# Performance work log

Hardware: AMD Instinct MI355X
Metric: run time of the kernel (lower is better)

## Reference

```python
import jax, jax.numpy as jnp
import numpy as np

E, W, S, Q, D = 256, 20, 5, 300, 512
ALPHA = 37.0  # hardcoded weight '37' in computeProto


def setup_inputs() -> dict:
    key = jax.random.key(0)
    k1, k2 = jax.random.split(key)
    x_shot = jax.random.normal(k1, (E, W, S, D), dtype=jnp.float32)
    x_query = jax.random.normal(k2, (E, Q, D), dtype=jnp.float32)
    temp = jnp.float32(10.0)
    return {"x_shot": x_shot, "x_query": x_query, "temp": temp}


def compute_proto(x_shot, x_query):
    # x_shot: [E, W, S, D], x_query: [E, Q, D]
    n_shot = x_shot.shape[2]
    shot_sum = x_shot.sum(axis=2)                      # [E, W, D]
    shot_mean = x_shot.mean(axis=2)                    # [E, W, D]
    # pairwise euclidean distance mean-vs-query: [E, W, Q]
    diff = shot_mean[:, :, None, :] - x_query[:, None, :, :]
    dist = jnp.sqrt(jnp.sum(diff * diff, axis=-1))
    weights = jax.nn.softmax(-dist, axis=-1)           # softmax over queries
    pooled = jnp.einsum('ewq,eqd->ewd', weights, x_query)  # [E, W, D]
    proto = (shot_sum + ALPHA * pooled) / (n_shot + ALPHA)
    return proto


def l2norm(x, axis=-1, eps=1e-12):
    n = jnp.sqrt(jnp.sum(x * x, axis=axis, keepdims=True))
    return x / jnp.maximum(n, eps)


def reference(x_shot, x_query, temp):
    proto = compute_proto(x_shot, x_query)             # [E, W, D]
    proto = l2norm(proto)
    q = l2norm(x_query)
    logits = temp * jnp.einsum('eqd,ewd->eqw', q, proto)  # [E, Q, W]
    return logits
```

## Files before the change

kernel.cpp:

```cpp
#include <hip/hip_runtime.h>
#include <math.h>

#define E_ 256
#define W_ 20
#define S_ 5
#define Q_ 300
#define D_ 512
#define ALPHA_ 37.0f
#define QCH 64
#define NCH 5
#define QPAD 304

typedef __attribute__((ext_vector_type(8))) short bf16x8;
typedef __attribute__((ext_vector_type(4))) float f32x4;
typedef __attribute__((ext_vector_type(4))) unsigned int u32x4;

#define OFF_SS   0
#define OFF_XQ   32768
#define OFF_BUF  98304
#define OFF_Q2   122624
#define OFF_M2   123904
#define OFF_RED  124032
#define LDS_BYTES 124672

__device__ __forceinline__ unsigned short f2bf(float x) {
    unsigned int u = __builtin_bit_cast(unsigned int, x);
    u += 0x7fffu + ((u >> 16) & 1u);
    return (unsigned short)(u >> 16);
}
__device__ __forceinline__ float bf2f(unsigned short h) {
    unsigned int u = ((unsigned int)h) << 16;
    return __builtin_bit_cast(float, u);
}

__device__ __forceinline__ bf16x8 ldfrag(const char* base, int row, int k0) {
    const int phys = (k0 >> 3) ^ (row & 7);
    return *reinterpret_cast<const bf16x8*>(base + row * 1024 + phys * 16);
}

__device__ __forceinline__ void stage_chunk(const float4* xq4, char* s_xq, float* s_q2,
                                            int c, int qcount, int tid, bool write_q2) {
    const int qr = tid >> 3;
    const int i  = tid & 7;
    const bool valid = qr < qcount;
    const int qg = c * QCH + qr;
    float q2 = 0.f;
    const float4* row4 = xq4 + (size_t)(valid ? qg : 0) * (D_ / 4);
    #pragma unroll
    for (int j = 0; j < 8; ++j) {
        const int ch = i + 8 * j;
        float4 a = valid ? row4[2 * ch]     : make_float4(0.f, 0.f, 0.f, 0.f);
        float4 b = valid ? row4[2 * ch + 1] : make_float4(0.f, 0.f, 0.f, 0.f);
        q2 += a.x * a.x + a.y * a.y + a.z * a.z + a.w * a.w
            + b.x * b.x + b.y * b.y + b.z * b.z + b.w * b.w;
        u32x4 v;
        v[0] = (unsigned int)f2bf(a.x) | ((unsigned int)f2bf(a.y) << 16);
        v[1] = (unsigned int)f2bf(a.z) | ((unsigned int)f2bf(a.w) << 16);
        v[2] = (unsigned int)f2bf(b.x) | ((unsigned int)f2bf(b.y) << 16);
        v[3] = (unsigned int)f2bf(b.z) | ((unsigned int)f2bf(b.w) << 16);
        *reinterpret_cast<u32x4*>(s_xq + qr * 1024 + ((ch ^ (qr & 7)) << 4)) = v;
    }
    if (write_q2) {
        q2 += __shfl_xor(q2, 1);
        q2 += __shfl_xor(q2, 2);
        q2 += __shfl_xor(q2, 4);
        if (i == 0) s_q2[qg] = valid ? q2 : 0.f;
    }
}

__global__ __launch_bounds__(512) void fused4(const float* __restrict__ xs,
                                              const float* __restrict__ xq,
                                              const float* __restrict__ temp_p,
                                              float* __restrict__ out) {
    extern __shared__ char smem[];
    char*  s_ss  = smem + OFF_SS;
    char*  s_xq  = smem + OFF_XQ;
    float* s_buf = (float*)(smem + OFF_BUF);
    float* s_q2  = (float*)(smem + OFF_Q2);
    float* s_m2  = (float*)(smem + OFF_M2);
    float* s_red = (float*)(smem + OFF_RED);

    const int e    = blockIdx.x;
    const int tid  = threadIdx.x;
    const int lane = tid & 63;
    const int wv   = tid >> 6;
    const int ln15 = lane & 15;
    const int hi   = lane >> 4;

    const float*  xse = xs + (size_t)e * (W_ * S_ * D_);
    const float*  xqe = xq + (size_t)e * (Q_ * D_);
    const float4* xq4 = (const float4*)xqe;
    const float   temp = *temp_p;

    for (int idx = tid; idx < 12 * 64; idx += 512) {
        const int row = 20 + (idx >> 6), ch = idx & 63;
        u32x4 z = {0u, 0u, 0u, 0u};
        *reinterpret_cast<u32x4*>(s_ss + row * 1024 + ch * 16) = z;
    }
    {
        const int chb = tid >> 3;
        #pragma unroll
        for (int w = 0; w < W_; ++w) {
            float a = 0.f;
            #pragma unroll
            for (int s = 0; s < S_; ++s) a += xse[(w * S_ + s) * D_ + tid];
            *(unsigned short*)(s_ss + w * 1024 + ((chb ^ (w & 7)) << 4) + (tid & 7) * 2) = f2bf(a);
        }
    }
    __syncthreads();

    for (int w = wv; w < W_; w += 8) {
        bf16x8 v = *reinterpret_cast<const bf16x8*>(s_ss + w * 1024 + ((lane ^ (w & 7)) << 4));
        float p = 0.f;
        #pragma unroll
        for (int j = 0; j < 8; ++j) { float f = bf2f((unsigned short)v[j]); p += f * f; }
        #pragma unroll
        for (int off = 32; off; off >>= 1) p += __shfl_xor(p, off);
        if (lane == 0) s_m2[w] = p * (1.f / (S_ * S_));
    }
    __syncthreads();

    for (int c = 0; c < NCH; ++c) {
        const int qcount = (c == 4) ? (Q_ - 4 * QCH) : QCH;
        stage_chunk(xq4, s_xq, s_q2, c, qcount, tid, true);
        __syncthreads();
        const int mtile = wv >> 2, ntile = wv & 3;
        f32x4 acc = {0.f, 0.f, 0.f, 0.f};
        const int arow = mtile * 16 + ln15;
        const int brow = ntile * 16 + ln15;
        #pragma unroll
        for (int k = 0; k < 16; ++k) {
            bf16x8 a = ldfrag(s_ss, arow, k * 32 + hi * 8);
            bf16x8 b = ldfrag(s_xq, brow, k * 32 + hi * 8);
            acc = __builtin_amdgcn_mfma_f32_16x16x32_bf16(a, b, acc, 0, 0, 0);
        }
        const int qloc = ntile * 16 + ln15;
        if (qloc < qcount) {
            const int qg = c * QCH + qloc;
            const float q2v = s_q2[qg];
            #pragma unroll
            for (int r = 0; r < 4; ++r) {
                const int w = mtile * 16 + hi * 4 + r;
                if (w < W_) {
                    float d2 = s_m2[w] + q2v - 0.4f * acc[r];
                    s_buf[w * QPAD + qg] = -sqrtf(fmaxf(d2, 0.f));
                }
            }
        }
        __syncthreads();
    }

    for (int w = wv; w < W_; w += 8) {
        float mx = -1e30f;
        for (int q = lane; q < Q_; q += 64) mx = fmaxf(mx, s_buf[w * QPAD + q]);
        #pragma unroll
        for (int off = 32; off; off >>= 1) mx = fmaxf(mx, __shfl_xor(mx, off));
        float sm = 0.f;
        for (int q = lane; q < Q_; q += 64) {
            float ex = __expf(s_buf[w * QPAD + q] - mx);
            s_buf[w * QPAD + q] = ex;
            sm += ex;
        }
        #pragma unroll
        for (int off = 32; off; off >>= 1) sm += __shfl_xor(sm, off);
        const float inv = 1.f / sm;
        for (int q = lane; q < Q_; q += 64) s_buf[w * QPAD + q] *= inv;
    }
    __syncthreads();

    {
        float pr[W_];
        #pragma unroll
        for (int w = 0; w < W_; ++w) pr[w] = 0.f;
        for (int q0 = 0; q0 < Q_; q0 += 4) {
            const float qv0 = xqe[(q0 + 0) * D_ + tid];
            const float qv1 = xqe[(q0 + 1) * D_ + tid];
            const float qv2 = xqe[(q0 + 2) * D_ + tid];
            const float qv3 = xqe[(q0 + 3) * D_ + tid];
            #pragma unroll
            for (int w = 0; w < W_; ++w) {
                const float4 wt = *reinterpret_cast<const float4*>(&s_buf[w * QPAD + q0]);
                pr[w] += wt.x * qv0 + wt.y * qv1 + wt.z * qv2 + wt.w * qv3;
            }
        }
        const int chb = tid >> 3;
        #pragma unroll
        for (int w = 0; w < W_; ++w) {
            unsigned short h =
                *(unsigned short*)(s_ss + w * 1024 + ((chb ^ (w & 7)) << 4) + (tid & 7) * 2);
            pr[w] = (bf2f(h) + ALPHA_ * pr[w]) * (1.f / (S_ + ALPHA_));
        }
        #pragma unroll
        for (int w = 0; w < W_; ++w) {
            float p = pr[w] * pr[w];
            #pragma unroll
            for (int off = 32; off; off >>= 1) p += __shfl_xor(p, off);
            if (lane == 0) s_red[wv * W_ + w] = p;
        }
        __syncthreads();
        if (tid < W_) {
            float p = 0.f;
            #pragma unroll
            for (int k = 0; k < 8; ++k) p += s_red[k * W_ + tid];
            s_m2[tid] = 1.f / fmaxf(sqrtf(p), 1e-12f);
        }
        __syncthreads();
        #pragma unroll
        for (int w = 0; w < W_; ++w) {
            *(unsigned short*)(s_ss + w * 1024 + ((chb ^ (w & 7)) << 4) + (tid & 7) * 2) =
                f2bf(pr[w] * s_m2[w]);
        }
        __syncthreads();
    }

    for (int c = 0; c < NCH; ++c) {
        const int qcount = (c == 4) ? (Q_ - 4 * QCH) : QCH;
        stage_chunk(xq4, s_xq, s_q2, c, qcount, tid, false);
        __syncthreads();
        const int mtile = wv >> 1, ntile = wv & 1;
        f32x4 acc = {0.f, 0.f, 0.f, 0.f};
        const int arow = mtile * 16 + ln15;
        const int brow = ntile * 16 + ln15;
        #pragma unroll
        for (int k = 0; k < 16; ++k) {
            bf16x8 a = ldfrag(s_xq, arow, k * 32 + hi * 8);
            bf16x8 b = ldfrag(s_ss, brow, k * 32 + hi * 8);
            acc = __builtin_amdgcn_mfma_f32_16x16x32_bf16(a, b, acc, 0, 0, 0);
        }
        const int w = ntile * 16 + ln15;
        if (w < W_) {
            #pragma unroll
            for (int r = 0; r < 4; ++r) {
                const int qloc = mtile * 16 + hi * 4 + r;
                if (qloc < qcount) {
                    const int qg = c * QCH + qloc;
                    const float scale = temp / fmaxf(sqrtf(s_q2[qg]), 1e-12f);
                    out[(size_t)e * (Q_ * W_) + qg * W_ + w] = scale * acc[r];
                }
            }
        }
        __syncthreads();
    }
}

extern "C" void kernel_launch(void* const* d_in, const int* in_sizes, int n_in,
                              void* d_out, int out_size, void* d_ws, size_t ws_size,
                              hipStream_t stream) {
    const float* xs = (const float*)d_in[0];
    const float* xq = (const float*)d_in[1];
    const float* tp = (const float*)d_in[2];
    hipFuncSetAttribute(reinterpret_cast<const void*>(fused4),
                        hipFuncAttributeMaxDynamicSharedMemorySize, LDS_BYTES);
    fused4<<<E_, 512, LDS_BYTES, stream>>>(xs, xq, tp, (float*)d_out);
}
```

Measured before the change: 120.3 us.

## Prefetch next query chunk into registers and vectorize shot-sum loads

```diff
diff --git a/kernel.cpp b/kernel.cpp
--- a/kernel.cpp
+++ b/kernel.cpp
@@ -13,6 +13,7 @@
 
 typedef __attribute__((ext_vector_type(8))) short bf16x8;
 typedef __attribute__((ext_vector_type(4))) float f32x4;
+typedef __attribute__((ext_vector_type(2))) unsigned int u32x2;
 typedef __attribute__((ext_vector_type(4))) unsigned int u32x4;
 
 #define OFF_SS   0
@@ -38,21 +39,36 @@
     return *reinterpret_cast<const bf16x8*>(base + row * 1024 + phys * 16);
 }
 
-__device__ __forceinline__ void stage_chunk(const float4* xq4, char* s_xq, float* s_q2,
-                                            int c, int qcount, int tid, bool write_q2) {
+__device__ __forceinline__ void stage_load(const float4* xq4, int c, int qcount,
+                                           int tid, float4* r) {
+    const int qr = tid >> 3;
+    const int i  = tid & 7;
+    const int qg = c * QCH + ((qr < qcount) ? qr : 0);
+    const float4* row4 = xq4 + (size_t)qg * (D_ / 4);
+    #pragma unroll
+    for (int j = 0; j < 8; ++j) {
+        const int ch = i + 8 * j;
+        r[2 * j]     = row4[2 * ch];
+        r[2 * j + 1] = row4[2 * ch + 1];
+    }
+}
+
+template <bool WQ2>
+__device__ __forceinline__ void stage_write(const float4* r, char* s_xq, float* s_q2,
+                                            int c, int qcount, int tid) {
     const int qr = tid >> 3;
     const int i  = tid & 7;
     const bool valid = qr < qcount;
-    const int qg = c * QCH + qr;
     float q2 = 0.f;
-    const float4* row4 = xq4 + (size_t)(valid ? qg : 0) * (D_ / 4);
     #pragma unroll
     for (int j = 0; j < 8; ++j) {
         const int ch = i + 8 * j;
-        float4 a = valid ? row4[2 * ch]     : make_float4(0.f, 0.f, 0.f, 0.f);
-        float4 b = valid ? row4[2 * ch + 1] : make_float4(0.f, 0.f, 0.f, 0.f);
-        q2 += a.x * a.x + a.y * a.y + a.z * a.z + a.w * a.w
-            + b.x * b.x + b.y * b.y + b.z * b.z + b.w * b.w;
+        float4 a = valid ? r[2 * j]     : make_float4(0.f, 0.f, 0.f, 0.f);
+        float4 b = valid ? r[2 * j + 1] : make_float4(0.f, 0.f, 0.f, 0.f);
+        if (WQ2) {
+            q2 += a.x * a.x + a.y * a.y + a.z * a.z + a.w * a.w
+                + b.x * b.x + b.y * b.y + b.z * b.z + b.w * b.w;
+        }
         u32x4 v;
         v[0] = (unsigned int)f2bf(a.x) | ((unsigned int)f2bf(a.y) << 16);
         v[1] = (unsigned int)f2bf(a.z) | ((unsigned int)f2bf(a.w) << 16);
@@ -60,15 +76,15 @@
         v[3] = (unsigned int)f2bf(b.z) | ((unsigned int)f2bf(b.w) << 16);
         *reinterpret_cast<u32x4*>(s_xq + qr * 1024 + ((ch ^ (qr & 7)) << 4)) = v;
     }
-    if (write_q2) {
+    if (WQ2) {
         q2 += __shfl_xor(q2, 1);
         q2 += __shfl_xor(q2, 2);
         q2 += __shfl_xor(q2, 4);
-        if (i == 0) s_q2[qg] = valid ? q2 : 0.f;
-    }
-}
-
-__global__ __launch_bounds__(512) void fused4(const float* __restrict__ xs,
+        if (i == 0) s_q2[c * QCH + qr] = valid ? q2 : 0.f;
+    }
+}
+
+__global__ __launch_bounds__(512) void fused5(const float* __restrict__ xs,
                                               const float* __restrict__ xq,
                                               const float* __restrict__ temp_p,
                                               float* __restrict__ out) {
@@ -92,20 +108,32 @@
     const float4* xq4 = (const float4*)xqe;
     const float   temp = *temp_p;
 
+    float4 buf[16];
+
+    stage_load(xq4, 0, QCH, tid, buf);
+
     for (int idx = tid; idx < 12 * 64; idx += 512) {
         const int row = 20 + (idx >> 6), ch = idx & 63;
         u32x4 z = {0u, 0u, 0u, 0u};
         *reinterpret_cast<u32x4*>(s_ss + row * 1024 + ch * 16) = z;
     }
-    {
-        const int chb = tid >> 3;
-        #pragma unroll
-        for (int w = 0; w < W_; ++w) {
-            float a = 0.f;
-            #pragma unroll
-            for (int s = 0; s < S_; ++s) a += xse[(w * S_ + s) * D_ + tid];
-            *(unsigned short*)(s_ss + w * 1024 + ((chb ^ (w & 7)) << 4) + (tid & 7) * 2) = f2bf(a);
-        }
+    #pragma unroll
+    for (int it = 0; it < 5; ++it) {
+        const int idx = it * 512 + tid;
+        const int w   = idx >> 7;
+        const int dq  = idx & 127;
+        const float4* p0 = reinterpret_cast<const float4*>(xse + (w * S_) * D_ + dq * 4);
+        float4 a = p0[0];
+        #pragma unroll
+        for (int s = 1; s < S_; ++s) {
+            const float4 t = p0[s * (D_ / 4)];
+            a.x += t.x; a.y += t.y; a.z += t.z; a.w += t.w;
+        }
+        u32x2 v;
+        v[0] = (unsigned int)f2bf(a.x) | ((unsigned int)f2bf(a.y) << 16);
+        v[1] = (unsigned int)f2bf(a.z) | ((unsigned int)f2bf(a.w) << 16);
+        *reinterpret_cast<u32x2*>(s_ss + w * 1024 + (((dq >> 1) ^ (w & 7)) << 4) +
+                                  (dq & 1) * 8) = v;
     }
     __syncthreads();
 
@@ -122,8 +150,11 @@
 
     for (int c = 0; c < NCH; ++c) {
         const int qcount = (c == 4) ? (Q_ - 4 * QCH) : QCH;
-        stage_chunk(xq4, s_xq, s_q2, c, qcount, tid, true);
-        __syncthreads();
+        stage_write<true>(buf, s_xq, s_q2, c, qcount, tid);
+        __syncthreads();
+        if (c + 1 < NCH)
+            stage_load(xq4, c + 1, (c + 1 == 4) ? (Q_ - 4 * QCH) : QCH, tid, buf);
+
         const int mtile = wv >> 2, ntile = wv & 3;
         f32x4 acc = {0.f, 0.f, 0.f, 0.f};
         const int arow = mtile * 16 + ln15;
@@ -168,6 +199,8 @@
     }
     __syncthreads();
 
+    stage_load(xq4, 0, QCH, tid, buf);
+
     {
         float pr[W_];
         #pragma unroll
@@ -215,8 +248,11 @@
 
     for (int c = 0; c < NCH; ++c) {
         const int qcount = (c == 4) ? (Q_ - 4 * QCH) : QCH;
-        stage_chunk(xq4, s_xq, s_q2, c, qcount, tid, false);
-        __syncthreads();
+        stage_write<false>(buf, s_xq, s_q2, c, qcount, tid);
+        __syncthreads();
+        if (c + 1 < NCH)
+            stage_load(xq4, c + 1, (c + 1 == 4) ? (Q_ - 4 * QCH) : QCH, tid, buf);
+
         const int mtile = wv >> 1, ntile = wv & 1;
         f32x4 acc = {0.f, 0.f, 0.f, 0.f};
         const int arow = mtile * 16 + ln15;
@@ -249,7 +285,7 @@
     const float* xs = (const float*)d_in[0];
     const float* xq = (const float*)d_in[1];
     const float* tp = (const float*)d_in[2];
-    hipFuncSetAttribute(reinterpret_cast<const void*>(fused4),
+    hipFuncSetAttribute(reinterpret_cast<const void*>(fused5),
                         hipFuncAttributeMaxDynamicSharedMemorySize, LDS_BYTES);
-    fused4<<<E_, 512, LDS_BYTES, stream>>>(xs, xq, tp, (float*)d_out);
-}
+    fused5<<<E_, 512, LDS_BYTES, stream>>>(xs, xq, tp, (float*)d_out);
+}
```

Result: faster. 109.0 us (-9.4%).
